# Kernel tuning notes

Hardware: AMD Instinct MI355X
Metric: run time of the kernel (lower is better)

The kernel has to match this reference:

```python
import jax, jax.numpy as jnp
import numpy as np

MARGIN = 0.5

def setup_inputs() -> dict:
    key = jax.random.key(0)
    k1, k2 = jax.random.split(key)
    logits = jax.random.normal(k1, (4096, 128), dtype=jnp.float32)
    labels = jax.random.randint(k2, (4096, 128), 0, 2, dtype=jnp.int32)
    return {"logits": logits, "labels": labels}

def reference(logits, labels):
    # pos/neg masks per row
    pos = labels > 0            # [B, D]
    neg = labels == 0           # [B, D]
    # pairwise relu(margin - (pos_score - neg_score)) over all (i, j) doc pairs
    diff = logits[:, :, None] - logits[:, None, :]          # [B, D, D]
    pl = jax.nn.relu(MARGIN - diff)                         # [B, D, D]
    pair_mask = (pos[:, :, None] & neg[:, None, :]).astype(logits.dtype)  # [B, D, D]
    row_sum = jnp.sum(pl * pair_mask, axis=(1, 2))          # [B]
    counts = jnp.sum(pair_mask, axis=(1, 2))                # [B]
    valid = counts > 0
    row_mean = jnp.where(valid, row_sum / jnp.maximum(counts, 1.0), 0.0)
    n_valid = jnp.sum(valid.astype(logits.dtype))
    # mean over rows that have at least one (pos, neg) pair; 0.0 if none
    return jnp.where(n_valid > 0, jnp.sum(row_mean) / jnp.maximum(n_valid, 1.0), 0.0)
```

## Files before the change

kernel.cpp:

```cpp
#include <hip/hip_runtime.h>

#define MARGIN 0.5f
#define NROWS 4096
#define D 128
#define BLK_WAVES 16
#define NBLK (NROWS / BLK_WAVES)

__global__ __launch_bounds__(1024) void mrl_row_kernel(
    const float* __restrict__ logits,
    const int*   __restrict__ labels,
    float2* __restrict__ partial)
{
    const int wave = threadIdx.x >> 6;
    const int lane = threadIdx.x & 63;
    const int row  = blockIdx.x * BLK_WAVES + wave;

    __shared__ float  s_neg[BLK_WAVES][132];
    __shared__ float  s_pos[BLK_WAVES][132];
    __shared__ float2 sw[BLK_WAVES];

    const float* lrow   = logits + (size_t)row * D;
    const int*   labrow = labels + (size_t)row * D;

    const int i0 = lane * 2;
    float2 lv = *reinterpret_cast<const float2*>(lrow + i0);
    int2   bv = *reinterpret_cast<const int2*>(labrow + i0);

    const bool n0 = (bv.x == 0), n1 = (bv.y == 0);
    const bool p0 = (bv.x > 0),  p1 = (bv.y > 0);

    const unsigned long long mn0 = __ballot(n0);
    const unsigned long long mn1 = __ballot(n1);
    const unsigned long long mp0 = __ballot(p0);
    const unsigned long long mp1 = __ballot(p1);
    const unsigned long long below = (1ull << lane) - 1ull;

    const int nneg = __popcll(mn0) + __popcll(mn1);
    const int npos = __popcll(mp0) + __popcll(mp1);

    if (n0) s_neg[wave][__popcll(mn0 & below)]                 = lv.x;
    if (n1) s_neg[wave][__popcll(mn0) + __popcll(mn1 & below)] = lv.y;
    if (p0) s_pos[wave][__popcll(mp0 & below)]                 = MARGIN - lv.x;
    if (p1) s_pos[wave][__popcll(mp0) + __popcll(mp1 & below)] = MARGIN - lv.y;

    if (lane < 4) s_neg[wave][nneg + lane] = -3.0e38f;

    __builtin_amdgcn_wave_barrier();

    const int nneg4 = (nneg + 3) >> 2;
    const float4* vp = reinterpret_cast<const float4*>(s_neg[wave]);

    float acc = 0.f;
    for (int p = lane; p < npos; p += 64) {
        const float c = s_pos[wave][p];
        float a = 0.f;
#pragma unroll 2
        for (int q = 0; q < nneg4; ++q) {
            float4 v = vp[q];
            a += fmaxf(v.x + c, 0.f);
            a += fmaxf(v.y + c, 0.f);
            a += fmaxf(v.z + c, 0.f);
            a += fmaxf(v.w + c, 0.f);
        }
        acc += a;
    }

    for (int off = 32; off > 0; off >>= 1)
        acc += __shfl_xor(acc, off);

    if (lane == 0) {
        const int cnt = npos * nneg;
        sw[wave] = (cnt > 0) ? make_float2(acc / (float)cnt, 1.f)
                             : make_float2(0.f, 0.f);
    }
    __syncthreads();

    if (wave == 0) {
        float2 t = (lane < BLK_WAVES) ? sw[lane] : make_float2(0.f, 0.f);
        for (int off = 8; off > 0; off >>= 1) {
            t.x += __shfl_xor(t.x, off);
            t.y += __shfl_xor(t.y, off);
        }
        if (lane == 0) partial[blockIdx.x] = t;
    }
}

__global__ __launch_bounds__(256) void mrl_reduce_kernel(
    const float2* __restrict__ partial,
    float* __restrict__ out)
{
    float2 t = partial[threadIdx.x];
    for (int off = 32; off > 0; off >>= 1) {
        t.x += __shfl_xor(t.x, off);
        t.y += __shfl_xor(t.y, off);
    }
    __shared__ float2 sw[4];
    const int wave = threadIdx.x >> 6;
    const int lane = threadIdx.x & 63;
    if (lane == 0) sw[wave] = t;
    __syncthreads();
    if (threadIdx.x == 0) {
        const float S = sw[0].x + sw[1].x + sw[2].x + sw[3].x;
        const float V = sw[0].y + sw[1].y + sw[2].y + sw[3].y;
        out[0] = (V > 0.f) ? S / V : 0.f;
    }
}

extern "C" void kernel_launch(void* const* d_in, const int* in_sizes, int n_in,
                              void* d_out, int out_size, void* d_ws, size_t ws_size,
                              hipStream_t stream) {
    const float* logits = (const float*)d_in[0];
    const int*   labels = (const int*)d_in[1];
    float* out = (float*)d_out;
    float2* partial = (float2*)d_ws;

    mrl_row_kernel<<<NBLK, 1024, 0, stream>>>(logits, labels, partial);
    mrl_reduce_kernel<<<1, 256, 0, stream>>>(partial, out);
}
```

Baseline: 12.18 us.

## Fuse final reduction into row kernel via last-block atomic ticket

Removes the second reduction kernel launch. Each block now writes its packed (sum, count) partial to a slot with an atomic exchange, then bumps a global ticket. The block that sees the ticket reach a multiple of NBLK does the final reduction over all slots. This saves a kernel launch and its dependency gap, at the cost of atomics and a ticket counter that persists across calls and relies on modular wraparound.

```diff
diff --git a/kernel.cpp b/kernel.cpp
--- a/kernel.cpp
+++ b/kernel.cpp
@@ -6,10 +6,12 @@
 #define BLK_WAVES 16
 #define NBLK (NROWS / BLK_WAVES)
 
-__global__ __launch_bounds__(1024) void mrl_row_kernel(
+__global__ __launch_bounds__(1024) void mrl_fused_kernel(
     const float* __restrict__ logits,
     const int*   __restrict__ labels,
-    float2* __restrict__ partial)
+    unsigned long long* __restrict__ slots,
+    unsigned int*       __restrict__ ticket,
+    float*              __restrict__ out)
 {
     const int wave = threadIdx.x >> 6;
     const int lane = threadIdx.x & 63;
@@ -18,6 +20,7 @@
     __shared__ float  s_neg[BLK_WAVES][132];
     __shared__ float  s_pos[BLK_WAVES][132];
     __shared__ float2 sw[BLK_WAVES];
+    __shared__ int    s_last;
 
     const float* lrow   = logits + (size_t)row * D;
     const int*   labrow = labels + (size_t)row * D;
@@ -75,33 +78,43 @@
     }
     __syncthreads();
 
-    if (wave == 0) {
-        float2 t = (lane < BLK_WAVES) ? sw[lane] : make_float2(0.f, 0.f);
-        for (int off = 8; off > 0; off >>= 1) {
-            t.x += __shfl_xor(t.x, off);
-            t.y += __shfl_xor(t.y, off);
-        }
-        if (lane == 0) partial[blockIdx.x] = t;
+    if (threadIdx.x == 0) {
+        float S = 0.f, V = 0.f;
+#pragma unroll
+        for (int w = 0; w < BLK_WAVES; ++w) { S += sw[w].x; V += sw[w].y; }
+
+        const unsigned long long packed =
+            ((unsigned long long)__float_as_uint(V) << 32) | __float_as_uint(S);
+
+        unsigned long long old = __hip_atomic_exchange(
+            &slots[blockIdx.x], packed, __ATOMIC_RELAXED, __HIP_MEMORY_SCOPE_AGENT);
+        asm volatile("s_waitcnt vmcnt(0)" :: "v"(old) : "memory");
+
+        const unsigned int t = __hip_atomic_fetch_add(
+            ticket, 1u, __ATOMIC_RELAXED, __HIP_MEMORY_SCOPE_AGENT);
+        s_last = (((t + 1u) & (NBLK - 1u)) == 0u) ? 1 : 0;
     }
-}
+    __syncthreads();
+    if (!s_last) return;
 
-__global__ __launch_bounds__(256) void mrl_reduce_kernel(
-    const float2* __restrict__ partial,
-    float* __restrict__ out)
-{
-    float2 t = partial[threadIdx.x];
+    float2 t = make_float2(0.f, 0.f);
+    if (threadIdx.x < NBLK) {
+        const unsigned long long v = __hip_atomic_load(
+            &slots[threadIdx.x], __ATOMIC_RELAXED, __HIP_MEMORY_SCOPE_AGENT);
+        t.x = __uint_as_float((unsigned int)(v & 0xffffffffull));
+        t.y = __uint_as_float((unsigned int)(v >> 32));
+    }
     for (int off = 32; off > 0; off >>= 1) {
         t.x += __shfl_xor(t.x, off);
         t.y += __shfl_xor(t.y, off);
     }
-    __shared__ float2 sw[4];
-    const int wave = threadIdx.x >> 6;
-    const int lane = threadIdx.x & 63;
+    __syncthreads();
     if (lane == 0) sw[wave] = t;
     __syncthreads();
     if (threadIdx.x == 0) {
-        const float S = sw[0].x + sw[1].x + sw[2].x + sw[3].x;
-        const float V = sw[0].y + sw[1].y + sw[2].y + sw[3].y;
+        float S = 0.f, V = 0.f;
+#pragma unroll
+        for (int w = 0; w < BLK_WAVES; ++w) { S += sw[w].x; V += sw[w].y; }
         out[0] = (V > 0.f) ? S / V : 0.f;
     }
 }
@@ -112,8 +125,8 @@
     const float* logits = (const float*)d_in[0];
     const int*   labels = (const int*)d_in[1];
     float* out = (float*)d_out;
-    float2* partial = (float2*)d_ws;
+    unsigned long long* slots  = (unsigned long long*)d_ws;
+    unsigned int*       ticket = (unsigned int*)(slots + NBLK);
 
-    mrl_row_kernel<<<NBLK, 1024, 0, stream>>>(logits, labels, partial);
-    mrl_reduce_kernel<<<1, 256, 0, stream>>>(partial, out);
+    mrl_fused_kernel<<<NBLK, 1024, 0, stream>>>(logits, labels, slots, ticket, out);
 }
```

New measurement: 13.90 us. 1.14x slower.
